# Kernel optimization log

Measured on AMD Instinct MI355X. Metric: run time of the kernel, lower is better.

The kernel has to match this reference:

```python
import jax, jax.numpy as jnp
import numpy as np

K = 49        # k_neighbors
EPS = 1e-5    # BatchNorm2d eps


def setup_inputs() -> dict:
    key = jax.random.key(0)
    ks = jax.random.split(key, 2)
    B, C, M, O = 64, 64, 32, 128
    X = jax.random.normal(ks[0], (B, C, M, M), dtype=jnp.float32)
    # conv1x1 weight (kaiming fan_out) flattened to (O, C); bias init 0
    W = jax.random.normal(ks[1], (O, C), dtype=jnp.float32) * (2.0 / O) ** 0.5
    b = jnp.zeros((O,), jnp.float32)
    gamma = jnp.ones((O,), jnp.float32)
    beta = jnp.zeros((O,), jnp.float32)
    run_mean = jnp.zeros((O,), jnp.float32)
    run_var = jnp.ones((O,), jnp.float32)
    return dict(X=X, W=W, b=b, gamma=gamma, beta=beta,
                run_mean=run_mean, run_var=run_var)


def _knn_aggregate(x):
    """x: (N, C) node features -> D^{-1/2} A D^{-1/2} x for the kNN graph."""
    N = x.shape[0]
    sq = jnp.sum(x * x, axis=1)
    d2 = sq[:, None] + sq[None, :] - 2.0 * (x @ x.T)
    dist = jnp.sqrt(jnp.maximum(d2, 0.0))              # torch.cdist (p=2)
    i = jnp.arange(N)
    dist = dist.at[i, i].set(jnp.inf)                  # fill_diagonal_(inf)
    _, knn = jax.lax.top_k(-dist, K)                   # (N, K) nearest indices
    # topk indices are distinct -> every row degree == K, and the column
    # normalizer uses the col node's row degree (also K), so
    # D^{-1/2} A D^{-1/2} x == mean of gathered neighbors.
    nb = x[knn]                                        # (N, K, C) gather
    return nb.sum(axis=1) / K


def reference(X, W, b, gamma, beta, run_mean, run_var):
    B, C, M, _ = X.shape
    N = M * M
    x = X.reshape(B, C, N).transpose(0, 2, 1)          # (B, N, C) nodes
    Z = jax.vmap(_knn_aggregate)(x)                    # (B, N, C) sparse GCN agg
    # 1x1 conv over the (M, M) grid == per-node linear map
    Fg = jnp.einsum('oc,bnc->bon', W, Z) + b[None, :, None]   # (B, O, N)
    Fg = jax.nn.relu(Fg)
    # BatchNorm2d with running stats (eval mode); Dropout2d is identity in eval
    inv = jax.lax.rsqrt(run_var + EPS)
    Fg = gamma[None, :, None] * (Fg - run_mean[None, :, None]) * inv[None, :, None] + beta[None, :, None]
    return Fg.mean(axis=2)                             # AdaptiveAvgPool2d(1) -> (B, O)
```

## Files before the change

### kernel.cpp

```cpp
#include <hip/hip_runtime.h>
#include <stdint.h>

#define BATCH 64
#define CDIM  64
#define NPTS  1024
#define ODIM  128
#define KNN   49
#define KNNP  52
#define BNEPS 1e-5f
#define ZPAD  72

typedef __attribute__((ext_vector_type(8))) short bf16x8;
typedef __attribute__((ext_vector_type(4))) float f32x4;
typedef union { bf16x8 v; uint32_t d[4]; } bfu;

__device__ __forceinline__ int mbcnt64(unsigned long long m) {
    return __builtin_amdgcn_mbcnt_hi((uint32_t)(m >> 32),
           __builtin_amdgcn_mbcnt_lo((uint32_t)m, 0));
}

__device__ __forceinline__ void bf16_split(float x, uint32_t& h, uint32_t& l) {
    uint32_t u = __float_as_uint(x);
    h = (u + 0x7FFFu + ((u >> 16) & 1u)) >> 16;
    float hf = __uint_as_float(h << 16);
    uint32_t ul = __float_as_uint(x - hf);
    l = (ul + 0x7FFFu + ((ul >> 16) & 1u)) >> 16;
}

#define O_XF   0
#define SZ_XF  (BATCH*64*2*64*8*4)
#define O_SQ   (O_XF + SZ_XF)
#define SZ_SQ  (BATCH*NPTS*4)
#define O_KNN  (O_SQ + SZ_SQ)
#define SZ_KNN (BATCH*NPTS*KNNP*4)
#define WS_NEED ((size_t)(O_KNN + SZ_KNN))

__global__ void gcn_init(const float* __restrict__ gamma, const float* __restrict__ beta,
                         const float* __restrict__ rmean, const float* __restrict__ rvar,
                         float* __restrict__ out) {
    int i = blockIdx.x * 256 + threadIdx.x;
    if (i < BATCH * ODIM) {
        int o = i & (ODIM - 1);
        out[i] = beta[o] - gamma[o] * rmean[o] * rsqrtf(rvar[o] + BNEPS);
    }
}

__global__ __launch_bounds__(256) void k0_split(const float* __restrict__ X,
                                                uint32_t* __restrict__ XF,
                                                float* __restrict__ sq,
                                                const float* __restrict__ gamma,
                                                const float* __restrict__ beta,
                                                const float* __restrict__ rmean,
                                                const float* __restrict__ rvar,
                                                float* __restrict__ out) {
    if (blockIdx.x < 32) {
        int i = blockIdx.x * 256 + threadIdx.x;
        int o = i & (ODIM - 1);
        out[i] = beta[o] - gamma[o] * rmean[o] * rsqrtf(rvar[o] + BNEPS);
    }
    const int b    = blockIdx.x >> 4;
    const int t16  = (blockIdx.x & 15) * 4 + (threadIdx.x >> 6);
    const int lane = threadIdx.x & 63;
    const int n    = t16 * 16 + (lane & 15);
    const int cg   = lane >> 4;
    const float* Xb = X + (size_t)b * CDIM * NPTS;
    float s = 0.f;
    for (int ks = 0; ks < 2; ks++) {
        uint32_t hi[4], lo[4];
#pragma unroll
        for (int dj = 0; dj < 4; dj++) {
            uint32_t hw[2], lw[2];
#pragma unroll
            for (int e = 0; e < 2; e++) {
                int c = ks * 32 + cg * 8 + dj * 2 + e;
                float x = Xb[(size_t)c * NPTS + n];
                s += x * x;
                bf16_split(x, hw[e], lw[e]);
            }
            hi[dj] = hw[0] | (hw[1] << 16);
            lo[dj] = lw[0] | (lw[1] << 16);
        }
        size_t entry = ((size_t)(b * 64 + t16) * 2 + ks) * 64 + lane;
        uint32_t* p = XF + entry * 8;
        *(uint4*)p       = make_uint4(hi[0], hi[1], hi[2], hi[3]);
        *(uint4*)(p + 4) = make_uint4(lo[0], lo[1], lo[2], lo[3]);
    }
    s += __shfl_xor(s, 16, 64);
    s += __shfl_xor(s, 32, 64);
    if (lane < 16) sq[b * NPTS + n] = s;
}

__global__ __launch_bounds__(512, 6) void k1_gram_select(const uint32_t* __restrict__ XF,
                                                         const float* __restrict__ sq,
                                                         int* __restrict__ knn) {
    __shared__ uint32_t s_pk[8 * 1024];
    const int b    = blockIdx.x >> 6;
    const int rt   = blockIdx.x & 63;
    const int wave = threadIdx.x >> 6, lane = threadIdx.x & 63;
    const int q = lane >> 4, l15 = lane & 15;

    bf16x8 ahi[2], alo[2];
#pragma unroll
    for (int ks = 0; ks < 2; ks++) {
        const uint32_t* p = XF + (((size_t)(b * 64 + rt) * 2 + ks) * 64 + lane) * 8;
        ahi[ks] = *(const bf16x8*)p;
        alo[ks] = *(const bf16x8*)(p + 4);
    }
    const float* sqb = sq + b * NPTS;

#pragma unroll
    for (int tt = 0; tt < 8; tt++) {
        const int t16 = wave * 8 + tt;
        f32x4 acc = {0.f, 0.f, 0.f, 0.f};
#pragma unroll
        for (int ks = 0; ks < 2; ks++) {
            const uint32_t* p = XF + (((size_t)(b * 64 + t16) * 2 + ks) * 64 + lane) * 8;
            bf16x8 bhi = *(const bf16x8*)p;
            bf16x8 blo = *(const bf16x8*)(p + 4);
            acc = __builtin_amdgcn_mfma_f32_16x16x32_bf16(ahi[ks], bhi, acc, 0, 0, 0);
            acc = __builtin_amdgcn_mfma_f32_16x16x32_bf16(alo[ks], bhi, acc, 0, 0, 0);
            acc = __builtin_amdgcn_mfma_f32_16x16x32_bf16(ahi[ks], blo, acc, 0, 0, 0);
        }
        const int col  = t16 * 16 + l15;
        const float sqv = sqb[col];
        uint32_t k16[4];
#pragma unroll
        for (int i = 0; i < 4; i++) {
            int row = q * 4 + i;
            float d = fmaf(-2.f, acc[i], sqv);
            if (col == rt * 16 + row) d = __uint_as_float(0x7F800000u);
            uint32_t u = __float_as_uint(d);
            uint32_t key = ((int)u < 0) ? ~u : (u | 0x80000000u);
            k16[i] = key >> 16;
        }
        const int p0 = 2 * q, p1 = 2 * q + 1;
        s_pk[p0 * 1024 + (col ^ ((p0 & 3) << 3))] = k16[0] | (k16[1] << 16);
        s_pk[p1 * 1024 + (col ^ ((p1 & 3) << 3))] = k16[2] | (k16[3] << 16);
    }
    __syncthreads();

    uint32_t k0r[16], k1r[16];
    {
        const int sw = (wave & 3) << 3;
#pragma unroll
        for (int tt = 0; tt < 16; tt++) {
            uint32_t pk = s_pk[wave * 1024 + ((tt * 64 + lane) ^ sw)];
            k0r[tt] = pk & 0xFFFFu;
            k1r[tt] = pk >> 16;
        }
    }

    uint32_t lo0, hi0, lo1, hi1;
    {
        uint32_t lm0 = k0r[0], lm1 = k1r[0];
#pragma unroll
        for (int tt = 1; tt < 16; tt++) {
            lm0 = k0r[tt] < lm0 ? k0r[tt] : lm0;
            lm1 = k1r[tt] < lm1 ? k1r[tt] : lm1;
        }
        uint32_t g0 = lm0, m0 = lm0, g1 = lm1, m1 = lm1;
#pragma unroll
        for (int off = 1; off < 64; off <<= 1) {
            uint32_t a0 = (uint32_t)__shfl_xor((int)g0, off, 64);
            uint32_t b0 = (uint32_t)__shfl_xor((int)m0, off, 64);
            uint32_t a1 = (uint32_t)__shfl_xor((int)g1, off, 64);
            uint32_t b1 = (uint32_t)__shfl_xor((int)m1, off, 64);
            g0 = a0 < g0 ? a0 : g0;  m0 = b0 > m0 ? b0 : m0;
            g1 = a1 < g1 ? a1 : g1;  m1 = b1 > m1 ? b1 : m1;
        }
        lo0 = g0; hi0 = m0;
        lo1 = g1; hi1 = m1;
    }

    for (int it = 0; it < 16; it++) {
        bool a0 = lo0 < hi0, a1 = lo1 < hi1;
        if (!a0 && !a1) break;
        uint32_t mid0 = (lo0 + hi0) >> 1;
        uint32_t mid1 = (lo1 + hi1) >> 1;
        int cnt0 = 0, cnt1 = 0;
#pragma unroll
        for (int tt = 0; tt < 16; tt++) {
            cnt0 += __popcll(__ballot(k0r[tt] <= mid0));
            cnt1 += __popcll(__ballot(k1r[tt] <= mid1));
        }
        if (a0) { if (cnt0 >= KNN) hi0 = mid0; else lo0 = mid0 + 1; }
        if (a1) { if (cnt1 >= KNN) hi1 = mid1; else lo1 = mid1 + 1; }
    }

#pragma unroll
    for (int r = 0; r < 2; r++) {
        const int row = wave * 2 + r;
        const uint32_t vstar = r ? lo1 : lo0;
        const uint32_t* k = r ? k1r : k0r;
        int total_lt = 0;
#pragma unroll
        for (int tt = 0; tt < 16; tt++)
            total_lt += __popcll(__ballot(k[tt] < vstar));
        int base_lt = 0, base_eq = total_lt;
        int* kout = knn + ((size_t)b * NPTS + rt * 16 + row) * KNNP;
#pragma unroll
        for (int tt = 0; tt < 16; tt++) {
            bool islt = k[tt] < vstar;
            bool iseq = k[tt] == vstar;
            unsigned long long mlt = __ballot(islt);
            unsigned long long meq = __ballot(iseq);
            if (mlt | meq) {
                int pos = islt ? (base_lt + mbcnt64(mlt)) : (base_eq + mbcnt64(meq));
                if (islt || (iseq && pos < KNN)) kout[pos] = tt * 64 + lane;
            }
            base_lt += __popcll(mlt);
            base_eq += __popcll(meq);
        }
    }
}

__global__ __launch_bounds__(256) void k2_mfma(const float* __restrict__ X,
                                               const int* __restrict__ knn,
                                               const float* __restrict__ W,
                                               const float* __restrict__ bias,
                                               const float* __restrict__ gamma,
                                               const float* __restrict__ rvar,
                                               float* __restrict__ out) {
    __shared__ __align__(16) uint32_t s_mem[(36864 + 2048) / 4];
    float*    XT8 = (float*)s_mem;
    uint16_t* ZFh = (uint16_t*)s_mem;
    uint16_t* ZFl = ZFh + 128 * ZPAD;
    float*    red = (float*)((uint8_t*)s_mem + 36864);

    const int b = blockIdx.x >> 3, nq = blockIdx.x & 7;
    const int t = threadIdx.x;
    const int rl = t >> 1, gg = t & 1;
    const int row = nq * 128 + rl;
    const int* kr = knn + ((size_t)b * NPTS + row) * KNNP;
    int4 j[13];
#pragma unroll
    for (int c = 0; c < 13; c++) j[c] = *(const int4*)&kr[c * 4];

    float4 zacc[8];
    for (int cg8 = 0; cg8 < 8; cg8++) {
        __syncthreads();
        const float* Xc = X + ((size_t)b * CDIM + cg8 * 8) * NPTS;
#pragma unroll
        for (int k4 = 0; k4 < 4; k4++) {
            int n = k4 * 256 + t;
#pragma unroll
            for (int g2 = 0; g2 < 2; g2++) {
                float4 v;
                v.x = Xc[(size_t)(g2 * 4 + 0) * NPTS + n];
                v.y = Xc[(size_t)(g2 * 4 + 1) * NPTS + n];
                v.z = Xc[(size_t)(g2 * 4 + 2) * NPTS + n];
                v.w = Xc[(size_t)(g2 * 4 + 3) * NPTS + n];
                int sl = (g2 ^ (n & 1)) << 2;
                *(float4*)&XT8[n * 8 + sl] = v;
            }
        }
        __syncthreads();
        float4 s = {0.f, 0.f, 0.f, 0.f};
#pragma unroll
        for (int c = 0; c < 12; c++) {
            int js[4] = {j[c].x, j[c].y, j[c].z, j[c].w};
#pragma unroll
            for (int e = 0; e < 4; e++) {
                int jj = js[e];
                float4 v = *(const float4*)&XT8[jj * 8 + ((gg ^ (jj & 1)) << 2)];
                s.x += v.x; s.y += v.y; s.z += v.z; s.w += v.w;
            }
        }
        {
            int jj = j[12].x;
            float4 v = *(const float4*)&XT8[jj * 8 + ((gg ^ (jj & 1)) << 2)];
            s.x += v.x; s.y += v.y; s.z += v.z; s.w += v.w;
        }
        zacc[cg8] = s;
    }
    __syncthreads();

#pragma unroll
    for (int cg8 = 0; cg8 < 8; cg8++) {
        const int c0 = cg8 * 8 + gg * 4;
        float v[4] = {zacc[cg8].x, zacc[cg8].y, zacc[cg8].z, zacc[cg8].w};
        uint32_t h[4], l[4];
#pragma unroll
        for (int e = 0; e < 4; e++) bf16_split(v[e], h[e], l[e]);
        uint2 hd = make_uint2(h[0] | (h[1] << 16), h[2] | (h[3] << 16));
        uint2 ld = make_uint2(l[0] | (l[1] << 16), l[2] | (l[3] << 16));
        *(uint2*)&ZFh[rl * ZPAD + c0] = hd;
        *(uint2*)&ZFl[rl * ZPAD + c0] = ld;
    }
    __syncthreads();

    const int wave = t >> 6, lane = t & 63;
    const int q = lane >> 4, l15 = lane & 15;
    bf16x8 zah[2][2], zal[2][2];
#pragma unroll
    for (int m2 = 0; m2 < 2; m2++) {
        const int m = (wave * 2 + m2) * 16 + l15;
#pragma unroll
        for (int kt = 0; kt < 2; kt++) {
            const int kb = kt * 32 + q * 8;
            zah[m2][kt] = *(const bf16x8*)&ZFh[m * ZPAD + kb];
            zal[m2][kt] = *(const bf16x8*)&ZFl[m * ZPAD + kb];
        }
    }
    const float inv49 = 1.f / KNN;
    float p[8];
#pragma unroll
    for (int nt = 0; nt < 8; nt++) {
        const int o = nt * 16 + l15;
        bfu wh[2], wl[2];
#pragma unroll
        for (int kt = 0; kt < 2; kt++) {
            const float* wp = W + (size_t)o * CDIM + kt * 32 + q * 8;
            float4 wa = *(const float4*)wp;
            float4 wb = *(const float4*)(wp + 4);
            float wv[8] = {wa.x, wa.y, wa.z, wa.w, wb.x, wb.y, wb.z, wb.w};
            uint32_t h[8], l[8];
#pragma unroll
            for (int e = 0; e < 8; e++) bf16_split(wv[e], h[e], l[e]);
#pragma unroll
            for (int dd = 0; dd < 4; dd++) {
                wh[kt].d[dd] = h[2 * dd] | (h[2 * dd + 1] << 16);
                wl[kt].d[dd] = l[2 * dd] | (l[2 * dd + 1] << 16);
            }
        }
        f32x4 acc0 = {0.f, 0.f, 0.f, 0.f};
        f32x4 acc1 = {0.f, 0.f, 0.f, 0.f};
#pragma unroll
        for (int kt = 0; kt < 2; kt++) {
            acc0 = __builtin_amdgcn_mfma_f32_16x16x32_bf16(zah[0][kt], wh[kt].v, acc0, 0, 0, 0);
            acc0 = __builtin_amdgcn_mfma_f32_16x16x32_bf16(zal[0][kt], wh[kt].v, acc0, 0, 0, 0);
            acc0 = __builtin_amdgcn_mfma_f32_16x16x32_bf16(zah[0][kt], wl[kt].v, acc0, 0, 0, 0);
            acc1 = __builtin_amdgcn_mfma_f32_16x16x32_bf16(zah[1][kt], wh[kt].v, acc1, 0, 0, 0);
            acc1 = __builtin_amdgcn_mfma_f32_16x16x32_bf16(zal[1][kt], wh[kt].v, acc1, 0, 0, 0);
            acc1 = __builtin_amdgcn_mfma_f32_16x16x32_bf16(zah[1][kt], wl[kt].v, acc1, 0, 0, 0);
        }
        const float bo = bias[o];
        float s = 0.f;
#pragma unroll
        for (int reg = 0; reg < 4; reg++) {
            s += fmaxf(fmaf(acc0[reg], inv49, bo), 0.f);
            s += fmaxf(fmaf(acc1[reg], inv49, bo), 0.f);
        }
        p[nt] = s;
    }
#pragma unroll
    for (int nt = 0; nt < 8; nt++) {
        p[nt] += __shfl_xor(p[nt], 16, 64);
        p[nt] += __shfl_xor(p[nt], 32, 64);
    }
    if (lane < 16) {
#pragma unroll
        for (int nt = 0; nt < 8; nt++)
            red[wave * 128 + nt * 16 + l15] = p[nt];
    }
    __syncthreads();
    if (t < 128) {
        float s = red[t] + red[128 + t] + red[256 + t] + red[384 + t];
        float scale = gamma[t] * rsqrtf(rvar[t] + BNEPS) * (1.f / NPTS);
        atomicAdd(&out[b * ODIM + t], s * scale);
    }
}

#define RTILE 8
#define APAD  1028
#define WPAD  132
#define POOLF (64 * WPAD)

__global__ __launch_bounds__(256) void gcn_main(
    const float* __restrict__ X, const float* __restrict__ W,
    const float* __restrict__ bias, const float* __restrict__ gamma,
    const float* __restrict__ rvar, float* __restrict__ out)
{
    __shared__ __align__(16) float s_pool[POOLF];
    __shared__ __align__(16) float s_fstage[4][APAD];
    __shared__ int   s_knn[RTILE][KNN];
    __shared__ float s_z[RTILE][CDIM];

    const int t = threadIdx.x;
    const int b = blockIdx.x >> 7;
    const int rtile = blockIdx.x & 127;
    const int r0 = rtile * RTILE;
    const float* Xb = X + (size_t)b * CDIM * NPTS;

    float acc[RTILE][4];
    float sqv[4];
#pragma unroll
    for (int r = 0; r < RTILE; r++)
#pragma unroll
        for (int u = 0; u < 4; u++) acc[r][u] = 0.f;
#pragma unroll
    for (int u = 0; u < 4; u++) sqv[u] = 0.f;

    for (int ch = 0; ch < 16; ch++) {
        const int c0 = ch * 4;
#pragma unroll
        for (int cc = 0; cc < 4; cc++) {
            float4 v = *(const float4*)(Xb + (size_t)(c0 + cc) * NPTS + 4 * t);
            *(float4*)&s_fstage[cc][4 * t] = v;
        }
        __syncthreads();
#pragma unroll
        for (int cc = 0; cc < 4; cc++) {
            float4 bv4 = *(const float4*)&s_fstage[cc][4 * t];
            float bv[4] = {bv4.x, bv4.y, bv4.z, bv4.w};
#pragma unroll
            for (int u = 0; u < 4; u++) sqv[u] += bv[u] * bv[u];
            const float* arow = Xb + (size_t)(c0 + cc) * NPTS + r0;
            float4 a0 = *(const float4*)(arow);
            float4 a1 = *(const float4*)(arow + 4);
            float av[8] = {a0.x, a0.y, a0.z, a0.w, a1.x, a1.y, a1.z, a1.w};
#pragma unroll
            for (int r = 0; r < RTILE; r++)
#pragma unroll
                for (int u = 0; u < 4; u++) acc[r][u] += av[r] * bv[u];
        }
        __syncthreads();
    }

    float* s_dist = s_pool;
#pragma unroll
    for (int r = 0; r < RTILE; r++) {
        const int rG = r0 + r;
        float d[4];
#pragma unroll
        for (int u = 0; u < 4; u++) {
            float dd = sqv[u] - 2.f * acc[r][u];
            d[u] = (4 * t + u == rG) ? __uint_as_float(0x7F800000u) : dd;
        }
        *(float4*)&s_dist[r * NPTS + 4 * t] = make_float4(d[0], d[1], d[2], d[3]);
    }
    __syncthreads();

    const int wave = t >> 6, lane = t & 63;
    const unsigned long long ltmask = (1ull << lane) - 1ull;
    for (int rr = 0; rr < 2; rr++) {
        const int row = wave * 2 + rr;
        unsigned key[16];
#pragma unroll
        for (int tt = 0; tt < 16; tt++) {
            unsigned u = __float_as_uint(s_dist[row * NPTS + tt * 64 + lane]);
            key[tt] = (u & 0x80000000u) ? ~u : (u | 0x80000000u);
        }
        unsigned lo = 0u, hi = 0xFFFFFFFFu;
        while (lo < hi) {
            unsigned mid = lo + ((hi - lo) >> 1);
            int cnt = 0;
#pragma unroll
            for (int tt = 0; tt < 16; tt++)
                cnt += __popcll(__ballot(key[tt] <= mid));
            if (cnt >= KNN) hi = mid; else lo = mid + 1;
        }
        const unsigned v49 = lo;
        int cntless = 0;
#pragma unroll
        for (int tt = 0; tt < 16; tt++)
            cntless += __popcll(__ballot(key[tt] < v49));
        const int need = KNN - cntless;
        int base = 0, eqtaken = 0;
#pragma unroll
        for (int tt = 0; tt < 16; tt++) {
            bool islt = key[tt] < v49;
            bool iseq = key[tt] == v49;
            unsigned long long meq = __ballot(iseq);
            int eqrank = eqtaken + __popcll(meq & ltmask);
            bool sel = islt || (iseq && (eqrank < need));
            unsigned long long msel = __ballot(sel);
            if (sel) {
                int pos = base + __popcll(msel & ltmask);
                s_knn[row][pos] = tt * 64 + lane;
            }
            base    += __popcll(msel);
            eqtaken += __popcll(meq);
        }
    }
    __syncthreads();

    float* astage = s_pool;
    float* s_redf = (float*)s_fstage;
    const int ar = t >> 5, acc8 = (t & 31) >> 2, ks = t & 3;
    for (int c0 = 0; c0 < CDIM; c0 += 8) {
#pragma unroll
        for (int qq = 0; qq < 8; qq++) {
            int if4 = qq * 256 + t;
            int cc = if4 >> 8, j4 = if4 & 255;
            float4 v = *(const float4*)(Xb + (size_t)(c0 + cc) * NPTS + 4 * j4);
            *(float4*)&astage[cc * APAD + 4 * j4] = v;
        }
        __syncthreads();
        float partial = 0.f;
        for (int k = ks; k < KNN; k += 4)
            partial += astage[acc8 * APAD + s_knn[ar][k]];
        s_redf[t] = partial;
        __syncthreads();
        if (t < 64) {
            int r = t >> 3, cc = t & 7;
            int bi = r * 32 + cc * 4;
            s_z[r][c0 + cc] = s_redf[bi] + s_redf[bi + 1] + s_redf[bi + 2] + s_redf[bi + 3];
        }
        __syncthreads();
    }

    float* wt = s_pool;
#pragma unroll 4
    for (int qq = 0; qq < 32; qq++) {
        int e = qq * 256 + t;
        int o = e >> 6, c = e & 63;
        wt[c * WPAD + o] = W[e];
    }
    __syncthreads();
    const int o = t & 127, rg = t >> 7;
    float facc[4] = {0.f, 0.f, 0.f, 0.f};
    for (int c = 0; c < CDIM; c += 4) {
        float w0 = wt[(c + 0) * WPAD + o], w1 = wt[(c + 1) * WPAD + o];
        float w2 = wt[(c + 2) * WPAD + o], w3 = wt[(c + 3) * WPAD + o];
#pragma unroll
        for (int qq = 0; qq < 4; qq++) {
            float4 zv = *(const float4*)&s_z[rg * 4 + qq][c];
            facc[qq] += w0 * zv.x + w1 * zv.y + w2 * zv.z + w3 * zv.w;
        }
    }
    const float bo = bias[o];
    float rsum = 0.f;
#pragma unroll
    for (int qq = 0; qq < 4; qq++) {
        float f = facc[qq] * (1.f / KNN) + bo;
        rsum += fmaxf(f, 0.f);
    }
    s_redf[t] = rsum;
    __syncthreads();
    if (t < 128) {
        float scale = gamma[t] * rsqrtf(rvar[t] + BNEPS) * (1.f / NPTS);
        atomicAdd(&out[b * ODIM + t], (s_redf[t] + s_redf[t + 128]) * scale);
    }
}

extern "C" void kernel_launch(void* const* d_in, const int* in_sizes, int n_in,
                              void* d_out, int out_size, void* d_ws, size_t ws_size,
                              hipStream_t stream) {
    const float* X     = (const float*)d_in[0];
    const float* W     = (const float*)d_in[1];
    const float* bias  = (const float*)d_in[2];
    const float* gamma = (const float*)d_in[3];
    const float* beta  = (const float*)d_in[4];
    const float* rmean = (const float*)d_in[5];
    const float* rvar  = (const float*)d_in[6];
    float* out = (float*)d_out;

    if (ws_size >= WS_NEED) {
        uint8_t* ws = (uint8_t*)d_ws;
        uint32_t* XF  = (uint32_t*)(ws + O_XF);
        float*    sqw = (float*)(ws + O_SQ);
        int*      knn = (int*)(ws + O_KNN);
        k0_split<<<BATCH * 16, 256, 0, stream>>>(X, XF, sqw, gamma, beta, rmean, rvar, out);
        k1_gram_select<<<BATCH * 64, 512, 0, stream>>>(XF, sqw, knn);
        k2_mfma<<<BATCH * 8, 256, 0, stream>>>(X, knn, W, bias, gamma, rvar, out);
    } else {
        gcn_init<<<(BATCH * ODIM + 255) / 256, 256, 0, stream>>>(gamma, beta, rmean, rvar, out);
        gcn_main<<<BATCH * (NPTS / RTILE), 256, 0, stream>>>(X, W, bias, gamma, rvar, out);
    }
}
```

Baseline: 254.2 us.

## Double-buffer X channel tiles in k2 and precompute split bf16 weights

The k2 gather stage now double-buffers the per-channel-group transposed X tile in shared memory. The next group is loaded while neighbors are summed from the current one, which removes one barrier per iteration and hides global load latency. The hi/lo bf16 split of W, previously redone by every k2 block, is computed once in spare k0 blocks into workspace and loaded directly as MFMA fragments. Shared memory per block rises to about 66KB, which can lower occupancy.

```diff
diff --git a/kernel.cpp b/kernel.cpp
--- a/kernel.cpp
+++ b/kernel.cpp
@@ -33,7 +33,9 @@
 #define SZ_SQ  (BATCH*NPTS*4)
 #define O_KNN  (O_SQ + SZ_SQ)
 #define SZ_KNN (BATCH*NPTS*KNNP*4)
-#define WS_NEED ((size_t)(O_KNN + SZ_KNN))
+#define O_WF   (O_KNN + SZ_KNN)
+#define SZ_WF  (2*16*64*16)
+#define WS_NEED ((size_t)(O_WF + SZ_WF))
 
 __global__ void gcn_init(const float* __restrict__ gamma, const float* __restrict__ beta,
                          const float* __restrict__ rmean, const float* __restrict__ rvar,
@@ -46,8 +48,11 @@
 }
 
 __global__ __launch_bounds__(256) void k0_split(const float* __restrict__ X,
+                                                const float* __restrict__ W,
                                                 uint32_t* __restrict__ XF,
                                                 float* __restrict__ sq,
+                                                uint32_t* __restrict__ WFh,
+                                                uint32_t* __restrict__ WFl,
                                                 const float* __restrict__ gamma,
                                                 const float* __restrict__ beta,
                                                 const float* __restrict__ rmean,
@@ -57,6 +62,20 @@
         int i = blockIdx.x * 256 + threadIdx.x;
         int o = i & (ODIM - 1);
         out[i] = beta[o] - gamma[o] * rmean[o] * rsqrtf(rvar[o] + BNEPS);
+    } else if (blockIdx.x < 36) {
+        int item = (blockIdx.x - 32) * 256 + threadIdx.x;
+        int e = item >> 6, ln = item & 63;
+        int nt = e >> 1, kt = e & 1;
+        int o = nt * 16 + (ln & 15);
+        int kc = kt * 32 + (ln >> 4) * 8;
+        const float* wp = W + (size_t)o * CDIM + kc;
+        uint32_t h[8], l[8];
+#pragma unroll
+        for (int jj = 0; jj < 8; jj++) bf16_split(wp[jj], h[jj], l[jj]);
+        *(uint4*)&WFh[item * 4] = make_uint4(h[0] | (h[1] << 16), h[2] | (h[3] << 16),
+                                             h[4] | (h[5] << 16), h[6] | (h[7] << 16));
+        *(uint4*)&WFl[item * 4] = make_uint4(l[0] | (l[1] << 16), l[2] | (l[3] << 16),
+                                             l[4] | (l[5] << 16), l[6] | (l[7] << 16));
     }
     const int b    = blockIdx.x >> 4;
     const int t16  = (blockIdx.x & 15) * 4 + (threadIdx.x >> 6);
@@ -216,16 +235,17 @@
 
 __global__ __launch_bounds__(256) void k2_mfma(const float* __restrict__ X,
                                                const int* __restrict__ knn,
-                                               const float* __restrict__ W,
+                                               const uint32_t* __restrict__ WFh,
+                                               const uint32_t* __restrict__ WFl,
                                                const float* __restrict__ bias,
                                                const float* __restrict__ gamma,
                                                const float* __restrict__ rvar,
                                                float* __restrict__ out) {
-    __shared__ __align__(16) uint32_t s_mem[(36864 + 2048) / 4];
-    float*    XT8 = (float*)s_mem;
+    __shared__ __align__(16) uint32_t s_mem[(65536 + 2048) / 4];
+    float*    XTb = (float*)s_mem;
     uint16_t* ZFh = (uint16_t*)s_mem;
     uint16_t* ZFl = ZFh + 128 * ZPAD;
-    float*    red = (float*)((uint8_t*)s_mem + 36864);
+    float*    red = (float*)((uint8_t*)s_mem + 65536);
 
     const int b = blockIdx.x >> 3, nq = blockIdx.x & 7;
     const int t = threadIdx.x;
@@ -237,9 +257,8 @@
     for (int c = 0; c < 13; c++) j[c] = *(const int4*)&kr[c * 4];
 
     float4 zacc[8];
-    for (int cg8 = 0; cg8 < 8; cg8++) {
-        __syncthreads();
-        const float* Xc = X + ((size_t)b * CDIM + cg8 * 8) * NPTS;
+    {
+        const float* Xc = X + (size_t)b * CDIM * NPTS;
 #pragma unroll
         for (int k4 = 0; k4 < 4; k4++) {
             int n = k4 * 256 + t;
@@ -251,10 +270,31 @@
                 v.z = Xc[(size_t)(g2 * 4 + 2) * NPTS + n];
                 v.w = Xc[(size_t)(g2 * 4 + 3) * NPTS + n];
                 int sl = (g2 ^ (n & 1)) << 2;
-                *(float4*)&XT8[n * 8 + sl] = v;
+                *(float4*)&XTb[n * 8 + sl] = v;
             }
         }
-        __syncthreads();
+    }
+    __syncthreads();
+    for (int cg8 = 0; cg8 < 8; cg8++) {
+        float* cur = XTb + (cg8 & 1) * 8192;
+        if (cg8 < 7) {
+            float* nxt = XTb + ((cg8 + 1) & 1) * 8192;
+            const float* Xc = X + ((size_t)b * CDIM + (cg8 + 1) * 8) * NPTS;
+#pragma unroll
+            for (int k4 = 0; k4 < 4; k4++) {
+                int n = k4 * 256 + t;
+#pragma unroll
+                for (int g2 = 0; g2 < 2; g2++) {
+                    float4 v;
+                    v.x = Xc[(size_t)(g2 * 4 + 0) * NPTS + n];
+                    v.y = Xc[(size_t)(g2 * 4 + 1) * NPTS + n];
+                    v.z = Xc[(size_t)(g2 * 4 + 2) * NPTS + n];
+                    v.w = Xc[(size_t)(g2 * 4 + 3) * NPTS + n];
+                    int sl = (g2 ^ (n & 1)) << 2;
+                    *(float4*)&nxt[n * 8 + sl] = v;
+                }
+            }
+        }
         float4 s = {0.f, 0.f, 0.f, 0.f};
 #pragma unroll
         for (int c = 0; c < 12; c++) {
@@ -262,18 +302,18 @@
 #pragma unroll
             for (int e = 0; e < 4; e++) {
                 int jj = js[e];
-                float4 v = *(const float4*)&XT8[jj * 8 + ((gg ^ (jj & 1)) << 2)];
+                float4 v = *(const float4*)&cur[jj * 8 + ((gg ^ (jj & 1)) << 2)];
                 s.x += v.x; s.y += v.y; s.z += v.z; s.w += v.w;
             }
         }
         {
             int jj = j[12].x;
-            float4 v = *(const float4*)&XT8[jj * 8 + ((gg ^ (jj & 1)) << 2)];
+            float4 v = *(const float4*)&cur[jj * 8 + ((gg ^ (jj & 1)) << 2)];
             s.x += v.x; s.y += v.y; s.z += v.z; s.w += v.w;
         }
         zacc[cg8] = s;
-    }
-    __syncthreads();
+        __syncthreads();
+    }
 
 #pragma unroll
     for (int cg8 = 0; cg8 < 8; cg8++) {
@@ -310,18 +350,9 @@
         bfu wh[2], wl[2];
 #pragma unroll
         for (int kt = 0; kt < 2; kt++) {
-            const float* wp = W + (size_t)o * CDIM + kt * 32 + q * 8;
-            float4 wa = *(const float4*)wp;
-            float4 wb = *(const float4*)(wp + 4);
-            float wv[8] = {wa.x, wa.y, wa.z, wa.w, wb.x, wb.y, wb.z, wb.w};
-            uint32_t h[8], l[8];
-#pragma unroll
-            for (int e = 0; e < 8; e++) bf16_split(wv[e], h[e], l[e]);
-#pragma unroll
-            for (int dd = 0; dd < 4; dd++) {
-                wh[kt].d[dd] = h[2 * dd] | (h[2 * dd + 1] << 16);
-                wl[kt].d[dd] = l[2 * dd] | (l[2 * dd + 1] << 16);
-            }
+            const int item = (nt * 2 + kt) * 64 + lane;
+            *(uint4*)wh[kt].d = *(const uint4*)&WFh[item * 4];
+            *(uint4*)wl[kt].d = *(const uint4*)&WFl[item * 4];
         }
         f32x4 acc0 = {0.f, 0.f, 0.f, 0.f};
         f32x4 acc1 = {0.f, 0.f, 0.f, 0.f};
@@ -551,9 +582,12 @@
         uint32_t* XF  = (uint32_t*)(ws + O_XF);
         float*    sqw = (float*)(ws + O_SQ);
         int*      knn = (int*)(ws + O_KNN);
-        k0_split<<<BATCH * 16, 256, 0, stream>>>(X, XF, sqw, gamma, beta, rmean, rvar, out);
+        uint32_t* WFh = (uint32_t*)(ws + O_WF);
+        uint32_t* WFl = WFh + 16 * 64 * 4;
+        k0_split<<<BATCH * 16, 256, 0, stream>>>(X, W, XF, sqw, WFh, WFl,
+                                                 gamma, beta, rmean, rvar, out);
         k1_gram_select<<<BATCH * 64, 512, 0, stream>>>(XF, sqw, knn);
-        k2_mfma<<<BATCH * 8, 256, 0, stream>>>(X, knn, W, bias, gamma, rvar, out);
+        k2_mfma<<<BATCH * 8, 256, 0, stream>>>(X, knn, WFh, WFl, bias, gamma, rvar, out);
     } else {
         gcn_init<<<(BATCH * ODIM + 255) / 256, 256, 0, stream>>>(gamma, beta, rmean, rvar, out);
         gcn_main<<<BATCH * (NPTS / RTILE), 256, 0, stream>>>(X, W, bias, gamma, rvar, out);
```

Measured after the change: 247.2 us. 2.7% less time.

## Replace kNN gather-sum with bitmask adjacency MFMA over bf16-split features

Applied to the files above, without the earlier changes.

The neighbor aggregation stops gathering 49 rows from LDS per point. Each block now builds a 128x1024 adjacency bitmask in shared memory with atomicOr and multiplies it against a pre-split hi/lo bf16 transposed copy of X using MFMA. That copy is produced in k0_split and stored in a new workspace region. The aggregation becomes a dense 0/1 matmul, which does much more arithmetic (the full 1024 columns instead of 49 neighbours) but uses matrix cores and regular loads in place of scattered LDS reads. It also adds workspace traffic, the LDS atomics, and per-iteration bitmask expansion.

```diff
diff --git a/kernel.cpp b/kernel.cpp
--- a/kernel.cpp
+++ b/kernel.cpp
@@ -33,7 +33,9 @@
 #define SZ_SQ  (BATCH*NPTS*4)
 #define O_KNN  (O_SQ + SZ_SQ)
 #define SZ_KNN (BATCH*NPTS*KNNP*4)
-#define WS_NEED ((size_t)(O_KNN + SZ_KNN))
+#define O_XFT  (O_KNN + SZ_KNN)
+#define SZ_XFT (BATCH*32*4*64*8*4)
+#define WS_NEED ((size_t)(O_XFT + SZ_XFT))
 
 __global__ void gcn_init(const float* __restrict__ gamma, const float* __restrict__ beta,
                          const float* __restrict__ rmean, const float* __restrict__ rvar,
@@ -48,6 +50,7 @@
 __global__ __launch_bounds__(256) void k0_split(const float* __restrict__ X,
                                                 uint32_t* __restrict__ XF,
                                                 float* __restrict__ sq,
+                                                uint32_t* __restrict__ XFT,
                                                 const float* __restrict__ gamma,
                                                 const float* __restrict__ beta,
                                                 const float* __restrict__ rmean,
@@ -59,7 +62,9 @@
         out[i] = beta[o] - gamma[o] * rmean[o] * rsqrtf(rvar[o] + BNEPS);
     }
     const int b    = blockIdx.x >> 4;
-    const int t16  = (blockIdx.x & 15) * 4 + (threadIdx.x >> 6);
+    const int g    = blockIdx.x & 15;
+    const int wv   = threadIdx.x >> 6;
+    const int t16  = g * 4 + wv;
     const int lane = threadIdx.x & 63;
     const int n    = t16 * 16 + (lane & 15);
     const int cg   = lane >> 4;
@@ -88,6 +93,23 @@
     s += __shfl_xor(s, 16, 64);
     s += __shfl_xor(s, 32, 64);
     if (lane < 16) sq[b * NPTS + n] = s;
+
+#pragma unroll
+    for (int sx = 0; sx < 2; sx++) {
+        int task = g * 8 + wv * 2 + sx;
+        int kt = task >> 2, ct = task & 3;
+        int c  = ct * 16 + (lane & 15);
+        int n0 = kt * 32 + (lane >> 4) * 8;
+        const float* xp = Xb + (size_t)c * NPTS + n0;
+        uint32_t h[8], l[8];
+#pragma unroll
+        for (int j = 0; j < 8; j++) bf16_split(xp[j], h[j], l[j]);
+        uint32_t* pp = XFT + ((((size_t)b * 32 + kt) * 4 + ct) * 64 + lane) * 8;
+        *(uint4*)pp       = make_uint4(h[0] | (h[1] << 16), h[2] | (h[3] << 16),
+                                       h[4] | (h[5] << 16), h[6] | (h[7] << 16));
+        *(uint4*)(pp + 4) = make_uint4(l[0] | (l[1] << 16), l[2] | (l[3] << 16),
+                                       l[4] | (l[5] << 16), l[6] | (l[7] << 16));
+    }
 }
 
 __global__ __launch_bounds__(512, 6) void k1_gram_select(const uint32_t* __restrict__ XF,
@@ -214,83 +236,93 @@
     }
 }
 
-__global__ __launch_bounds__(256) void k2_mfma(const float* __restrict__ X,
-                                               const int* __restrict__ knn,
-                                               const float* __restrict__ W,
-                                               const float* __restrict__ bias,
-                                               const float* __restrict__ gamma,
-                                               const float* __restrict__ rvar,
-                                               float* __restrict__ out) {
-    __shared__ __align__(16) uint32_t s_mem[(36864 + 2048) / 4];
-    float*    XT8 = (float*)s_mem;
-    uint16_t* ZFh = (uint16_t*)s_mem;
-    uint16_t* ZFl = ZFh + 128 * ZPAD;
-    float*    red = (float*)((uint8_t*)s_mem + 36864);
-
+__global__ __launch_bounds__(256) void k2_agg(const uint32_t* __restrict__ XFT,
+                                              const int* __restrict__ knn,
+                                              const float* __restrict__ W,
+                                              const float* __restrict__ bias,
+                                              const float* __restrict__ gamma,
+                                              const float* __restrict__ rvar,
+                                              float* __restrict__ out) {
+    __shared__ uint32_t bm[128][33];
+    __shared__ __align__(16) uint16_t ZFh[128 * ZPAD];
+    __shared__ __align__(16) uint16_t ZFl[128 * ZPAD];
+    __shared__ float red[512];
     const int b = blockIdx.x >> 3, nq = blockIdx.x & 7;
     const int t = threadIdx.x;
-    const int rl = t >> 1, gg = t & 1;
-    const int row = nq * 128 + rl;
-    const int* kr = knn + ((size_t)b * NPTS + row) * KNNP;
-    int4 j[13];
-#pragma unroll
-    for (int c = 0; c < 13; c++) j[c] = *(const int4*)&kr[c * 4];
-
-    float4 zacc[8];
-    for (int cg8 = 0; cg8 < 8; cg8++) {
-        __syncthreads();
-        const float* Xc = X + ((size_t)b * CDIM + cg8 * 8) * NPTS;
-#pragma unroll
-        for (int k4 = 0; k4 < 4; k4++) {
-            int n = k4 * 256 + t;
-#pragma unroll
-            for (int g2 = 0; g2 < 2; g2++) {
-                float4 v;
-                v.x = Xc[(size_t)(g2 * 4 + 0) * NPTS + n];
-                v.y = Xc[(size_t)(g2 * 4 + 1) * NPTS + n];
-                v.z = Xc[(size_t)(g2 * 4 + 2) * NPTS + n];
-                v.w = Xc[(size_t)(g2 * 4 + 3) * NPTS + n];
-                int sl = (g2 ^ (n & 1)) << 2;
-                *(float4*)&XT8[n * 8 + sl] = v;
-            }
-        }
-        __syncthreads();
-        float4 s = {0.f, 0.f, 0.f, 0.f};
-#pragma unroll
-        for (int c = 0; c < 12; c++) {
-            int js[4] = {j[c].x, j[c].y, j[c].z, j[c].w};
-#pragma unroll
-            for (int e = 0; e < 4; e++) {
-                int jj = js[e];
-                float4 v = *(const float4*)&XT8[jj * 8 + ((gg ^ (jj & 1)) << 2)];
-                s.x += v.x; s.y += v.y; s.z += v.z; s.w += v.w;
-            }
-        }
-        {
-            int jj = j[12].x;
-            float4 v = *(const float4*)&XT8[jj * 8 + ((gg ^ (jj & 1)) << 2)];
-            s.x += v.x; s.y += v.y; s.z += v.z; s.w += v.w;
-        }
-        zacc[cg8] = s;
-    }
-    __syncthreads();
-
-#pragma unroll
-    for (int cg8 = 0; cg8 < 8; cg8++) {
-        const int c0 = cg8 * 8 + gg * 4;
-        float v[4] = {zacc[cg8].x, zacc[cg8].y, zacc[cg8].z, zacc[cg8].w};
-        uint32_t h[4], l[4];
-#pragma unroll
-        for (int e = 0; e < 4; e++) bf16_split(v[e], h[e], l[e]);
-        uint2 hd = make_uint2(h[0] | (h[1] << 16), h[2] | (h[3] << 16));
-        uint2 ld = make_uint2(l[0] | (l[1] << 16), l[2] | (l[3] << 16));
-        *(uint2*)&ZFh[rl * ZPAD + c0] = hd;
-        *(uint2*)&ZFl[rl * ZPAD + c0] = ld;
-    }
-    __syncthreads();
-
     const int wave = t >> 6, lane = t & 63;
     const int q = lane >> 4, l15 = lane & 15;
+
+    {
+        uint32_t* bf = &bm[0][0];
+#pragma unroll
+        for (int i = 0; i < 17; i++) {
+            int idx = i * 256 + t;
+            if (idx < 4224) bf[idx] = 0u;
+        }
+    }
+    __syncthreads();
+    {
+        const int row = t >> 1, gg = t & 1;
+        const int* kr = knn + ((size_t)b * NPTS + nq * 128 + row) * KNNP;
+        int4 j[13];
+#pragma unroll
+        for (int c = 0; c < 13; c++) j[c] = *(const int4*)&kr[c * 4];
+        if (gg == 0) {
+#pragma unroll
+            for (int c = 0; c < 6; c++) {
+                int js[4] = {j[c].x, j[c].y, j[c].z, j[c].w};
+#pragma unroll
+                for (int e = 0; e < 4; e++)
+                    atomicOr(&bm[row][js[e] >> 5], 1u << (js[e] & 31));
+            }
+        } else {
+#pragma unroll
+            for (int c = 6; c < 12; c++) {
+                int js[4] = {j[c].x, j[c].y, j[c].z, j[c].w};
+#pragma unroll
+                for (int e = 0; e < 4; e++)
+                    atomicOr(&bm[row][js[e] >> 5], 1u << (js[e] & 31));
+            }
+            atomicOr(&bm[row][j[12].x >> 5], 1u << (j[12].x & 31));
+        }
+    }
+    __syncthreads();
+
+    const int ct = wave;
+    f32x4 acc[8];
+#pragma unroll
+    for (int mt = 0; mt < 8; mt++) acc[mt] = (f32x4){0.f, 0.f, 0.f, 0.f};
+    for (int kt = 0; kt < 32; kt++) {
+        const uint32_t* p = XFT + ((((size_t)b * 32 + kt) * 4 + ct) * 64 + lane) * 8;
+        bf16x8 bhi = *(const bf16x8*)p;
+        bf16x8 blo = *(const bf16x8*)(p + 4);
+#pragma unroll
+        for (int mt = 0; mt < 8; mt++) {
+            uint32_t byte = (bm[mt * 16 + l15][kt] >> (q * 8)) & 0xFFu;
+            bfu a;
+            a.d[0] = ((byte & 1u)  ? 0x3F80u : 0u) | ((byte & 2u)   ? 0x3F800000u : 0u);
+            a.d[1] = ((byte & 4u)  ? 0x3F80u : 0u) | ((byte & 8u)   ? 0x3F800000u : 0u);
+            a.d[2] = ((byte & 16u) ? 0x3F80u : 0u) | ((byte & 32u)  ? 0x3F800000u : 0u);
+            a.d[3] = ((byte & 64u) ? 0x3F80u : 0u) | ((byte & 128u) ? 0x3F800000u : 0u);
+            acc[mt] = __builtin_amdgcn_mfma_f32_16x16x32_bf16(a.v, bhi, acc[mt], 0, 0, 0);
+            acc[mt] = __builtin_amdgcn_mfma_f32_16x16x32_bf16(a.v, blo, acc[mt], 0, 0, 0);
+        }
+    }
+
+#pragma unroll
+    for (int mt = 0; mt < 8; mt++) {
+#pragma unroll
+        for (int reg = 0; reg < 4; reg++) {
+            int r = mt * 16 + q * 4 + reg;
+            int c = ct * 16 + l15;
+            uint32_t h, l;
+            bf16_split(acc[mt][reg], h, l);
+            ZFh[r * ZPAD + c] = (uint16_t)h;
+            ZFl[r * ZPAD + c] = (uint16_t)l;
+        }
+    }
+    __syncthreads();
+
     bf16x8 zah[2][2], zal[2][2];
 #pragma unroll
     for (int m2 = 0; m2 < 2; m2++) {
@@ -551,9 +583,11 @@
         uint32_t* XF  = (uint32_t*)(ws + O_XF);
         float*    sqw = (float*)(ws + O_SQ);
         int*      knn = (int*)(ws + O_KNN);
-        k0_split<<<BATCH * 16, 256, 0, stream>>>(X, XF, sqw, gamma, beta, rmean, rvar, out);
+        uint32_t* XFT = (uint32_t*)(ws + O_XFT);
+        k0_split<<<BATCH * 16, 256, 0, stream>>>(X, XF, sqw, XFT,
+                                                 gamma, beta, rmean, rvar, out);
         k1_gram_select<<<BATCH * 64, 512, 0, stream>>>(XF, sqw, knn);
-        k2_mfma<<<BATCH * 8, 256, 0, stream>>>(X, knn, W, bias, gamma, rvar, out);
+        k2_agg<<<BATCH * 8, 256, 0, stream>>>(XFT, knn, W, bias, gamma, rvar, out);
     } else {
         gcn_init<<<(BATCH * ODIM + 255) / 256, 256, 0, stream>>>(gamma, beta, rmean, rvar, out);
         gcn_main<<<BATCH * (NPTS / RTILE), 256, 0, stream>>>(X, W, bias, gamma, rvar, out);
```

Result: faster. 242.8 us (-4.5%).
